# Performance work log

Measured on AMD Instinct MI355X. Metric: run time of the kernel, lower is better.

Reference implementation:

```python
import jax, jax.numpy as jnp
import numpy as np

B, D, K, A, P = 4096, 512, 128, 32, 16  # batch, theta dim, mixture comps, alpha dim, hutchinson probes


def setup_inputs() -> dict:
    key = jax.random.key(0)
    k1, k2, k3, k4 = jax.random.split(key, 4)
    thetas = jax.random.normal(k1, (B, D), dtype=jnp.float32)
    alpha = jax.random.normal(k2, (K, A), dtype=jnp.float32)
    W = jax.random.normal(k3, (A, D), dtype=jnp.float32) / jnp.sqrt(jnp.float32(A))
    v_int = jax.random.randint(k4, (P, B, D), 0, 2, dtype=jnp.int32)  # -> Rademacher via 2v-1
    return {"thetas": thetas, "alpha": alpha, "W": W, "v_int": v_int,
            "N_dataset": 100000, "K_alpha_samples": K}


def _log_density(thetas, alpha, W, N_dataset, K_alpha):
    # Tempered Gaussian mixture: mu_k = alpha_k @ W;
    # logp_b = (N/(N+1)) * (logsumexp_k -0.5||theta_b - mu_k||^2 - log K)
    mu = alpha @ W                                        # [K, D]
    # ||t - mu||^2 expanded to avoid a [B,K,D] intermediate
    sq = (jnp.sum(thetas * thetas, -1, keepdims=True)
          - 2.0 * thetas @ mu.T
          + jnp.sum(mu * mu, -1)[None, :])                # [B, K]
    temper = jnp.float32(N_dataset) / (jnp.float32(N_dataset) + 1.0)
    return temper * (jax.nn.logsumexp(-0.5 * sq, axis=1) - jnp.log(jnp.float32(K_alpha)))


def reference(thetas, alpha, W, v_int, N_dataset, K_alpha_samples):
    v = (2 * v_int - 1).astype(thetas.dtype)              # [P, B, D] Rademacher

    def logp_sum(t):
        return jnp.sum(_log_density(t, alpha, W, N_dataset, K_alpha_samples))

    score = jax.grad(logp_sum)                            # gradiente wrt thetas
    g = score(thetas)                                     # [B, D]

    # Hutchinson trace of the per-sample Hessian via forward-over-reverse HVPs,
    # batched over probes (fuses the torch per-probe autograd.grad loop).
    def hvp(vi):
        return jax.jvp(score, (thetas,), (vi,))[1]        # [B, D]

    Hv = jax.vmap(hvp)(v)                                 # [P, B, D]
    traces = jnp.mean(jnp.sum(v * Hv, axis=-1), axis=0)   # [B]

    loss = 0.5 * jnp.sum(g * g, axis=-1) + traces         # [B]
    return jnp.mean(loss)
```

## Files before the change

kernel.cpp:

```cpp
#include <hip/hip_runtime.h>
#include <hip/hip_bf16.h>
#include <stdint.h>

#define Bsz 4096
#define Dn  512
#define Kn  128
#define Pn  16
#define An  32
#define TB  16

typedef __attribute__((ext_vector_type(4))) float  floatx4;
typedef __attribute__((ext_vector_type(8))) short  shortx8;

__device__ unsigned short g_mu_bf[Kn * Dn];
__device__ unsigned short g_mu_t[Dn * Kn];
__device__ float          g_munorm[Kn];
__device__ float          g_w[Bsz * Kn];

__device__ __forceinline__ unsigned short f2bf(float x) {
    union { float f; uint32_t u; } v; v.f = x;
    uint32_t u = v.u;
    uint32_t r = (u + 0x7FFFu + ((u >> 16) & 1u)) >> 16;
    return (unsigned short)r;
}

__device__ __forceinline__ float rowsum16(float x) {
    x += __int_as_float(__builtin_amdgcn_update_dpp(0, __float_as_int(x), 0xB1, 0xF, 0xF, false));
    x += __int_as_float(__builtin_amdgcn_update_dpp(0, __float_as_int(x), 0x4E, 0xF, 0xF, false));
    x += __int_as_float(__builtin_amdgcn_update_dpp(0, __float_as_int(x), 0x124, 0xF, 0xF, false));
    x += __int_as_float(__builtin_amdgcn_update_dpp(0, __float_as_int(x), 0x128, 0xF, 0xF, false));
    return x;
}

__global__ __launch_bounds__(256) void k_mu(const float* __restrict__ alpha,
                                            const float* __restrict__ W,
                                            float* __restrict__ out) {
    __shared__ float al[An];
    __shared__ float red[4];
    int k = blockIdx.x, t = threadIdx.x;
    if (k == 0 && t == 0) *out = 0.f;
    if (t < An) al[t] = alpha[k * An + t];
    __syncthreads();
    int d0 = t, d1 = t + 256;
    float a0 = 0.f, a1 = 0.f;
#pragma unroll
    for (int a = 0; a < An; ++a) {
        float av = al[a];
        a0 = fmaf(av, W[a * Dn + d0], a0);
        a1 = fmaf(av, W[a * Dn + d1], a1);
    }
    unsigned short h0 = f2bf(a0), h1 = f2bf(a1);
    g_mu_bf[k * Dn + d0] = h0;  g_mu_bf[k * Dn + d1] = h1;
    g_mu_t[d0 * Kn + k] = h0;   g_mu_t[d1 * Kn + k] = h1;
    float nrm = a0 * a0 + a1 * a1;
#pragma unroll
    for (int msk = 1; msk < 64; msk <<= 1) nrm += __shfl_xor(nrm, msk);
    if ((t & 63) == 0) red[t >> 6] = nrm;
    __syncthreads();
    if (t == 0) g_munorm[k] = red[0] + red[1] + red[2] + red[3];
}

__global__ __launch_bounds__(512) void k_w(const float* __restrict__ thetas,
                                           const int* __restrict__ Np,
                                           float* __restrict__ out) {
    __shared__ short vt[TB][520];
    __shared__ float S_l[TB][132];
    __shared__ float w_l[TB][132];
    __shared__ short wbf[TB][136];
    __shared__ float part8[8][TB];
    __shared__ float thn[TB];
    __shared__ float SwS[TB];

    const int tid = threadIdx.x;
    const int lane = tid & 63;
    const int wv = tid >> 6;
    const int m = lane & 15;
    const int q = lane >> 4;
    const int b0 = blockIdx.x * TB;

    const float Nf = (float)(*Np);
    const float temper = Nf / (Nf + 1.0f);

    const int kcol = wv * 16 + m;
    shortx8 mufrag[16];
    {
        const unsigned short* mb = g_mu_bf + (size_t)kcol * Dn + q * 8;
#pragma unroll
        for (int dc = 0; dc < 16; ++dc)
            mufrag[dc] = *(const shortx8*)(mb + dc * 32);
    }

    const int r = tid >> 5;
    const int c0 = (tid & 31) * 16;
    {
        const float4* tg = (const float4*)(thetas + (size_t)(b0 + r) * Dn + c0);
        float tn = 0.f;
#pragma unroll
        for (int j = 0; j < 4; ++j) {
            float4 f = tg[j];
            tn += f.x * f.x + f.y * f.y + f.z * f.z + f.w * f.w;
            short4 h;
            h.x = (short)f2bf(f.x); h.y = (short)f2bf(f.y);
            h.z = (short)f2bf(f.z); h.w = (short)f2bf(f.w);
            *(short4*)&vt[r][c0 + j * 4] = h;
        }
#pragma unroll
        for (int msk = 1; msk < 32; msk <<= 1) tn += __shfl_xor(tn, msk);
        if ((tid & 31) == 0) thn[r] = tn;
    }
    __syncthreads();

    {
        floatx4 acc = {0.f, 0.f, 0.f, 0.f};
#pragma unroll
        for (int dc = 0; dc < 16; ++dc) {
            shortx8 a = *(const shortx8*)&vt[m][dc * 32 + q * 8];
            acc = __builtin_amdgcn_mfma_f32_16x16x32_bf16(a, mufrag[dc], acc, 0, 0, 0);
        }
#pragma unroll
        for (int i = 0; i < 4; ++i) S_l[q * 4 + i][kcol] = acc[i];
    }
    __syncthreads();

    {
        const int b = tid >> 5, s = tid & 31;
        float l[4];
        float mx = -3.4e38f;
        float tnb = thn[b];
#pragma unroll
        for (int j = 0; j < 4; ++j) {
            int k = s + 32 * j;
            l[j] = -0.5f * (tnb - 2.f * S_l[b][k] + g_munorm[k]);
            mx = fmaxf(mx, l[j]);
        }
#pragma unroll
        for (int msk = 1; msk < 32; msk <<= 1) mx = fmaxf(mx, __shfl_xor(mx, msk));
        float se = 0.f, ses = 0.f;
        float e[4];
#pragma unroll
        for (int j = 0; j < 4; ++j) {
            int k = s + 32 * j;
            e[j] = __expf(l[j] - mx);
            se += e[j];
            ses += e[j] * S_l[b][k];
        }
#pragma unroll
        for (int msk = 1; msk < 32; msk <<= 1) { se += __shfl_xor(se, msk); ses += __shfl_xor(ses, msk); }
        float inv = 1.f / se;
#pragma unroll
        for (int j = 0; j < 4; ++j) {
            int k = s + 32 * j;
            float wvv = e[j] * inv;
            w_l[b][k] = wvv;
            wbf[b][k] = (short)f2bf(wvv);
            g_w[(size_t)(b0 + b) * Kn + k] = wvv;
        }
        if (s == 0) SwS[b] = ses * inv;
    }
    __syncthreads();

    {
        float sg[4] = {0.f, 0.f, 0.f, 0.f};
#pragma unroll
        for (int ct = 0; ct < 4; ++ct) {
            const unsigned short* mt = g_mu_t + (size_t)(wv * 64 + ct * 16 + m) * Kn + q * 8;
            floatx4 acc = {0.f, 0.f, 0.f, 0.f};
#pragma unroll
            for (int kc = 0; kc < 4; ++kc) {
                shortx8 a = *(const shortx8*)&wbf[m][kc * 32 + q * 8];
                shortx8 bfr = *(const shortx8*)(mt + kc * 32);
                acc = __builtin_amdgcn_mfma_f32_16x16x32_bf16(a, bfr, acc, 0, 0, 0);
            }
#pragma unroll
            for (int i = 0; i < 4; ++i) sg[i] += acc[i] * acc[i];
        }
#pragma unroll
        for (int i = 0; i < 4; ++i) sg[i] = rowsum16(sg[i]);
        if (m == 0) {
#pragma unroll
            for (int i = 0; i < 4; ++i) part8[wv][q * 4 + i] = sg[i];
        }
    }
    __syncthreads();

    if (tid < TB) {
        float wGw = 0.f;
#pragma unroll
        for (int w8 = 0; w8 < 8; ++w8) wGw += part8[w8][tid];
        float res = 0.5f * temper * temper * (wGw - 2.f * SwS[tid] + thn[tid])
                    - temper * (float)Dn;
#pragma unroll
        for (int msk = 1; msk < 16; msk <<= 1) res += __shfl_xor(res, msk);
        if (tid == 0) atomicAdd(out, res * (1.0f / (float)Bsz));
    }
}

__global__ __launch_bounds__(1024, 4) void k_probe(const int* __restrict__ v_int,
                                                   const int* __restrict__ Np,
                                                   float* __restrict__ out) {
    __shared__ __align__(16) unsigned short mu_l[Kn * Dn];
    __shared__ float w_l[TB][132];
    __shared__ float partial[16];

    const int tid = threadIdx.x;
    const int lane = tid & 63;
    const int wv = tid >> 6;
    const int m = lane & 15;
    const int q = lane >> 4;
    const int bt = blockIdx.x;
    const int r0 = bt * TB;

    const float Nf = (float)(*Np);
    const float temper = Nf / (Nf + 1.0f);

    {
        const int4* src = (const int4*)g_mu_bf;
#pragma unroll
        for (int i = 0; i < 8; ++i) {
            int c = i * 1024 + tid;
            int row = c >> 6;
            int off = (c & 63) * 16;
            int4 val = src[c];
            *(int4*)((char*)mu_l + row * 1024 + (off ^ ((row & 7) << 4))) = val;
        }
    }
    if (tid < 512) {
        int row = tid >> 5, c = (tid & 31) * 4;
        float4 w4 = *(const float4*)(g_w + (size_t)(r0 + row) * Kn + c);
        *(float4*)&w_l[row][c] = w4;
    }
    __syncthreads();

    const size_t PB = (size_t)Bsz * Dn;
    const char* vg = (const char*)(v_int + (size_t)wv * PB + (size_t)(r0 + m) * Dn) + q * 32;

    int4 vb[4][2];
#pragma unroll
    for (int c = 0; c < 4; ++c) {
        vb[c][0] = *(const int4*)(vg + c * 128);
        vb[c][1] = *(const int4*)(vg + c * 128 + 16);
    }

    floatx4 acc[8];
#pragma unroll
    for (int kt = 0; kt < 8; ++kt) acc[kt] = (floatx4){0.f, 0.f, 0.f, 0.f};

    const int swz = (m & 7) << 4;
#pragma unroll
    for (int dc = 0; dc < 16; ++dc) {
        int4 w0 = vb[dc & 3][0], w1 = vb[dc & 3][1];
        if (dc < 12) {
            vb[dc & 3][0] = *(const int4*)(vg + (dc + 4) * 128);
            vb[dc & 3][1] = *(const int4*)(vg + (dc + 4) * 128 + 16);
        }
        union { uint32_t u[4]; shortx8 s; } af;
        af.u[0] = 0xBF80BF80u ^ ((uint32_t)w0.x << 15) ^ ((uint32_t)w0.y << 31);
        af.u[1] = 0xBF80BF80u ^ ((uint32_t)w0.z << 15) ^ ((uint32_t)w0.w << 31);
        af.u[2] = 0xBF80BF80u ^ ((uint32_t)w1.x << 15) ^ ((uint32_t)w1.y << 31);
        af.u[3] = 0xBF80BF80u ^ ((uint32_t)w1.z << 15) ^ ((uint32_t)w1.w << 31);
        const int boff = dc * 64 + q * 16;
#pragma unroll
        for (int kt = 0; kt < 8; ++kt) {
            shortx8 bf = *(const shortx8*)((const char*)mu_l
                              + (kt * 16 + m) * 1024 + (boff ^ swz));
            acc[kt] = __builtin_amdgcn_mfma_f32_16x16x32_bf16(af.s, bf, acc[kt], 0, 0, 0);
        }
    }

    float contrib = 0.f;
#pragma unroll
    for (int i = 0; i < 4; ++i) {
        float s1 = 0.f, s2 = 0.f;
#pragma unroll
        for (int kt = 0; kt < 8; ++kt) {
            float T = acc[kt][i];
            float ww = w_l[q * 4 + i][kt * 16 + m];
            s1 = fmaf(ww * T, T, s1);
            s2 = fmaf(ww, T, s2);
        }
        s1 = rowsum16(s1);
        s2 = rowsum16(s2);
        contrib += s1 - s2 * s2;
    }
    if (m != 0) contrib = 0.f;
    contrib += __shfl_xor(contrib, 16);
    contrib += __shfl_xor(contrib, 32);
    if (lane == 0) partial[wv] = contrib;
    __syncthreads();
    if (tid == 0) {
        float t = 0.f;
#pragma unroll
        for (int i = 0; i < 16; ++i) t += partial[i];
        atomicAdd(out, t * temper * (1.0f / (float)Pn) * (1.0f / (float)Bsz));
    }
}

extern "C" void kernel_launch(void* const* d_in, const int* in_sizes, int n_in,
                              void* d_out, int out_size, void* d_ws, size_t ws_size,
                              hipStream_t stream) {
    const float* thetas = (const float*)d_in[0];
    const float* alpha  = (const float*)d_in[1];
    const float* W      = (const float*)d_in[2];
    const int*   v_int  = (const int*)d_in[3];
    const int*   Np     = (const int*)d_in[4];
    (void)d_ws; (void)ws_size;

    float* out = (float*)d_out;
    k_mu   <<<dim3(Kn),  dim3(256),  0, stream>>>(alpha, W, out);
    k_w    <<<dim3(256), dim3(512),  0, stream>>>(thetas, Np, out);
    k_probe<<<dim3(256), dim3(1024), 0, stream>>>(v_int, Np, out);
}
```

Before: 223.2 us.

## Fuse mixture-weight kernel into probe kernel and deepen v_int prefetch

Merges the k_w kernel, which computes softmax weights, the score norm and the mean term, into k_probe. The fused kernel reuses the mu tile already staged in shared memory instead of reading it again from global memory, and drops the global g_w round trip and one kernel launch. The v_int prefetch depth grows from 4 to 6 chunks and is issued before the weight computation, so its latency overlaps that work. The cost is higher register pressure under the 1024-thread, 4-block launch bounds, and half the waves sit idle during the fused weight phase.

```diff
diff --git a/kernel.cpp b/kernel.cpp
--- a/kernel.cpp
+++ b/kernel.cpp
@@ -15,7 +15,6 @@
 __device__ unsigned short g_mu_bf[Kn * Dn];
 __device__ unsigned short g_mu_t[Dn * Kn];
 __device__ float          g_munorm[Kn];
-__device__ float          g_w[Bsz * Kn];
 
 __device__ __forceinline__ unsigned short f2bf(float x) {
     union { float f; uint32_t u; } v; v.f = x;
@@ -60,146 +59,17 @@
     if (t == 0) g_munorm[k] = red[0] + red[1] + red[2] + red[3];
 }
 
-__global__ __launch_bounds__(512) void k_w(const float* __restrict__ thetas,
-                                           const int* __restrict__ Np,
-                                           float* __restrict__ out) {
-    __shared__ short vt[TB][520];
+__global__ __launch_bounds__(1024, 4) void k_probe(const float* __restrict__ thetas,
+                                                   const int* __restrict__ v_int,
+                                                   const int* __restrict__ Np,
+                                                   float* __restrict__ out) {
+    __shared__ __align__(16) unsigned short mu_l[Kn * Dn];
     __shared__ float S_l[TB][132];
     __shared__ float w_l[TB][132];
     __shared__ short wbf[TB][136];
     __shared__ float part8[8][TB];
     __shared__ float thn[TB];
     __shared__ float SwS[TB];
-
-    const int tid = threadIdx.x;
-    const int lane = tid & 63;
-    const int wv = tid >> 6;
-    const int m = lane & 15;
-    const int q = lane >> 4;
-    const int b0 = blockIdx.x * TB;
-
-    const float Nf = (float)(*Np);
-    const float temper = Nf / (Nf + 1.0f);
-
-    const int kcol = wv * 16 + m;
-    shortx8 mufrag[16];
-    {
-        const unsigned short* mb = g_mu_bf + (size_t)kcol * Dn + q * 8;
-#pragma unroll
-        for (int dc = 0; dc < 16; ++dc)
-            mufrag[dc] = *(const shortx8*)(mb + dc * 32);
-    }
-
-    const int r = tid >> 5;
-    const int c0 = (tid & 31) * 16;
-    {
-        const float4* tg = (const float4*)(thetas + (size_t)(b0 + r) * Dn + c0);
-        float tn = 0.f;
-#pragma unroll
-        for (int j = 0; j < 4; ++j) {
-            float4 f = tg[j];
-            tn += f.x * f.x + f.y * f.y + f.z * f.z + f.w * f.w;
-            short4 h;
-            h.x = (short)f2bf(f.x); h.y = (short)f2bf(f.y);
-            h.z = (short)f2bf(f.z); h.w = (short)f2bf(f.w);
-            *(short4*)&vt[r][c0 + j * 4] = h;
-        }
-#pragma unroll
-        for (int msk = 1; msk < 32; msk <<= 1) tn += __shfl_xor(tn, msk);
-        if ((tid & 31) == 0) thn[r] = tn;
-    }
-    __syncthreads();
-
-    {
-        floatx4 acc = {0.f, 0.f, 0.f, 0.f};
-#pragma unroll
-        for (int dc = 0; dc < 16; ++dc) {
-            shortx8 a = *(const shortx8*)&vt[m][dc * 32 + q * 8];
-            acc = __builtin_amdgcn_mfma_f32_16x16x32_bf16(a, mufrag[dc], acc, 0, 0, 0);
-        }
-#pragma unroll
-        for (int i = 0; i < 4; ++i) S_l[q * 4 + i][kcol] = acc[i];
-    }
-    __syncthreads();
-
-    {
-        const int b = tid >> 5, s = tid & 31;
-        float l[4];
-        float mx = -3.4e38f;
-        float tnb = thn[b];
-#pragma unroll
-        for (int j = 0; j < 4; ++j) {
-            int k = s + 32 * j;
-            l[j] = -0.5f * (tnb - 2.f * S_l[b][k] + g_munorm[k]);
-            mx = fmaxf(mx, l[j]);
-        }
-#pragma unroll
-        for (int msk = 1; msk < 32; msk <<= 1) mx = fmaxf(mx, __shfl_xor(mx, msk));
-        float se = 0.f, ses = 0.f;
-        float e[4];
-#pragma unroll
-        for (int j = 0; j < 4; ++j) {
-            int k = s + 32 * j;
-            e[j] = __expf(l[j] - mx);
-            se += e[j];
-            ses += e[j] * S_l[b][k];
-        }
-#pragma unroll
-        for (int msk = 1; msk < 32; msk <<= 1) { se += __shfl_xor(se, msk); ses += __shfl_xor(ses, msk); }
-        float inv = 1.f / se;
-#pragma unroll
-        for (int j = 0; j < 4; ++j) {
-            int k = s + 32 * j;
-            float wvv = e[j] * inv;
-            w_l[b][k] = wvv;
-            wbf[b][k] = (short)f2bf(wvv);
-            g_w[(size_t)(b0 + b) * Kn + k] = wvv;
-        }
-        if (s == 0) SwS[b] = ses * inv;
-    }
-    __syncthreads();
-
-    {
-        float sg[4] = {0.f, 0.f, 0.f, 0.f};
-#pragma unroll
-        for (int ct = 0; ct < 4; ++ct) {
-            const unsigned short* mt = g_mu_t + (size_t)(wv * 64 + ct * 16 + m) * Kn + q * 8;
-            floatx4 acc = {0.f, 0.f, 0.f, 0.f};
-#pragma unroll
-            for (int kc = 0; kc < 4; ++kc) {
-                shortx8 a = *(const shortx8*)&wbf[m][kc * 32 + q * 8];
-                shortx8 bfr = *(const shortx8*)(mt + kc * 32);
-                acc = __builtin_amdgcn_mfma_f32_16x16x32_bf16(a, bfr, acc, 0, 0, 0);
-            }
-#pragma unroll
-            for (int i = 0; i < 4; ++i) sg[i] += acc[i] * acc[i];
-        }
-#pragma unroll
-        for (int i = 0; i < 4; ++i) sg[i] = rowsum16(sg[i]);
-        if (m == 0) {
-#pragma unroll
-            for (int i = 0; i < 4; ++i) part8[wv][q * 4 + i] = sg[i];
-        }
-    }
-    __syncthreads();
-
-    if (tid < TB) {
-        float wGw = 0.f;
-#pragma unroll
-        for (int w8 = 0; w8 < 8; ++w8) wGw += part8[w8][tid];
-        float res = 0.5f * temper * temper * (wGw - 2.f * SwS[tid] + thn[tid])
-                    - temper * (float)Dn;
-#pragma unroll
-        for (int msk = 1; msk < 16; msk <<= 1) res += __shfl_xor(res, msk);
-        if (tid == 0) atomicAdd(out, res * (1.0f / (float)Bsz));
-    }
-}
-
-__global__ __launch_bounds__(1024, 4) void k_probe(const int* __restrict__ v_int,
-                                                   const int* __restrict__ Np,
-                                                   float* __restrict__ out) {
-    __shared__ __align__(16) unsigned short mu_l[Kn * Dn];
-    __shared__ float w_l[TB][132];
     __shared__ float partial[16];
 
     const int tid = threadIdx.x;
@@ -212,6 +82,7 @@
 
     const float Nf = (float)(*Np);
     const float temper = Nf / (Nf + 1.0f);
+    const int swz = (m & 7) << 4;
 
     {
         const int4* src = (const int4*)g_mu_bf;
@@ -224,34 +95,125 @@
             *(int4*)((char*)mu_l + row * 1024 + (off ^ ((row & 7) << 4))) = val;
         }
     }
-    if (tid < 512) {
-        int row = tid >> 5, c = (tid & 31) * 4;
-        float4 w4 = *(const float4*)(g_w + (size_t)(r0 + row) * Kn + c);
-        *(float4*)&w_l[row][c] = w4;
-    }
-    __syncthreads();
 
     const size_t PB = (size_t)Bsz * Dn;
     const char* vg = (const char*)(v_int + (size_t)wv * PB + (size_t)(r0 + m) * Dn) + q * 32;
-
-    int4 vb[4][2];
-#pragma unroll
-    for (int c = 0; c < 4; ++c) {
+    int4 vb[6][2];
+#pragma unroll
+    for (int c = 0; c < 6; ++c) {
         vb[c][0] = *(const int4*)(vg + c * 128);
         vb[c][1] = *(const int4*)(vg + c * 128 + 16);
     }
+    __syncthreads();
+
+    if (wv < 8) {
+        const float* tg = thetas + (size_t)(r0 + m) * Dn + q * 8;
+        floatx4 acc = {0.f, 0.f, 0.f, 0.f};
+        float tn = 0.f;
+#pragma unroll
+        for (int dc = 0; dc < 16; ++dc) {
+            float4 f0 = *(const float4*)(tg + dc * 32);
+            float4 f1 = *(const float4*)(tg + dc * 32 + 4);
+            tn += f0.x * f0.x + f0.y * f0.y + f0.z * f0.z + f0.w * f0.w
+                + f1.x * f1.x + f1.y * f1.y + f1.z * f1.z + f1.w * f1.w;
+            union { uint32_t u[4]; shortx8 s; } af;
+            af.u[0] = (uint32_t)f2bf(f0.x) | ((uint32_t)f2bf(f0.y) << 16);
+            af.u[1] = (uint32_t)f2bf(f0.z) | ((uint32_t)f2bf(f0.w) << 16);
+            af.u[2] = (uint32_t)f2bf(f1.x) | ((uint32_t)f2bf(f1.y) << 16);
+            af.u[3] = (uint32_t)f2bf(f1.z) | ((uint32_t)f2bf(f1.w) << 16);
+            shortx8 bf = *(const shortx8*)((const char*)mu_l
+                              + (wv * 16 + m) * 1024 + ((dc * 64 + q * 16) ^ swz));
+            acc = __builtin_amdgcn_mfma_f32_16x16x32_bf16(af.s, bf, acc, 0, 0, 0);
+        }
+#pragma unroll
+        for (int i = 0; i < 4; ++i) S_l[q * 4 + i][wv * 16 + m] = acc[i];
+        tn += __shfl_xor(tn, 16);
+        tn += __shfl_xor(tn, 32);
+        if (wv == 0 && q == 0) thn[m] = tn;
+    }
+    __syncthreads();
+
+    if (tid < 512) {
+        const int b = tid >> 5, s = tid & 31;
+        float l[4];
+        float mx = -3.4e38f;
+        float tnb = thn[b];
+#pragma unroll
+        for (int j = 0; j < 4; ++j) {
+            int k = s + 32 * j;
+            l[j] = -0.5f * (tnb - 2.f * S_l[b][k] + g_munorm[k]);
+            mx = fmaxf(mx, l[j]);
+        }
+#pragma unroll
+        for (int msk = 1; msk < 32; msk <<= 1) mx = fmaxf(mx, __shfl_xor(mx, msk));
+        float se = 0.f, ses = 0.f;
+        float e[4];
+#pragma unroll
+        for (int j = 0; j < 4; ++j) {
+            int k = s + 32 * j;
+            e[j] = __expf(l[j] - mx);
+            se += e[j];
+            ses += e[j] * S_l[b][k];
+        }
+#pragma unroll
+        for (int msk = 1; msk < 32; msk <<= 1) { se += __shfl_xor(se, msk); ses += __shfl_xor(ses, msk); }
+        float inv = 1.f / se;
+#pragma unroll
+        for (int j = 0; j < 4; ++j) {
+            int k = s + 32 * j;
+            float wvv = e[j] * inv;
+            w_l[b][k] = wvv;
+            wbf[b][k] = (short)f2bf(wvv);
+        }
+        if (s == 0) SwS[b] = ses * inv;
+    }
+    __syncthreads();
+
+    if (wv < 8) {
+        float sg[4] = {0.f, 0.f, 0.f, 0.f};
+#pragma unroll
+        for (int ct = 0; ct < 4; ++ct) {
+            const unsigned short* mt = g_mu_t + (size_t)(wv * 64 + ct * 16 + m) * Kn + q * 8;
+            floatx4 acc = {0.f, 0.f, 0.f, 0.f};
+#pragma unroll
+            for (int kc = 0; kc < 4; ++kc) {
+                shortx8 a = *(const shortx8*)&wbf[m][kc * 32 + q * 8];
+                shortx8 bfr = *(const shortx8*)(mt + kc * 32);
+                acc = __builtin_amdgcn_mfma_f32_16x16x32_bf16(a, bfr, acc, 0, 0, 0);
+            }
+#pragma unroll
+            for (int i = 0; i < 4; ++i) sg[i] += acc[i] * acc[i];
+        }
+#pragma unroll
+        for (int i = 0; i < 4; ++i) sg[i] = rowsum16(sg[i]);
+        if (m == 0) {
+#pragma unroll
+            for (int i = 0; i < 4; ++i) part8[wv][q * 4 + i] = sg[i];
+        }
+    }
+    __syncthreads();
+
+    if (tid < TB) {
+        float wGw = 0.f;
+#pragma unroll
+        for (int w8 = 0; w8 < 8; ++w8) wGw += part8[w8][tid];
+        float res = 0.5f * temper * temper * (wGw - 2.f * SwS[tid] + thn[tid])
+                    - temper * (float)Dn;
+#pragma unroll
+        for (int msk = 1; msk < 16; msk <<= 1) res += __shfl_xor(res, msk);
+        if (tid == 0) atomicAdd(out, res * (1.0f / (float)Bsz));
+    }
 
     floatx4 acc[8];
 #pragma unroll
     for (int kt = 0; kt < 8; ++kt) acc[kt] = (floatx4){0.f, 0.f, 0.f, 0.f};
 
-    const int swz = (m & 7) << 4;
 #pragma unroll
     for (int dc = 0; dc < 16; ++dc) {
-        int4 w0 = vb[dc & 3][0], w1 = vb[dc & 3][1];
-        if (dc < 12) {
-            vb[dc & 3][0] = *(const int4*)(vg + (dc + 4) * 128);
-            vb[dc & 3][1] = *(const int4*)(vg + (dc + 4) * 128 + 16);
+        int4 w0 = vb[dc % 6][0], w1 = vb[dc % 6][1];
+        if (dc < 10) {
+            vb[dc % 6][0] = *(const int4*)(vg + (dc + 6) * 128);
+            vb[dc % 6][1] = *(const int4*)(vg + (dc + 6) * 128 + 16);
         }
         union { uint32_t u[4]; shortx8 s; } af;
         af.u[0] = 0xBF80BF80u ^ ((uint32_t)w0.x << 15) ^ ((uint32_t)w0.y << 31);
@@ -307,6 +269,5 @@
 
     float* out = (float*)d_out;
     k_mu   <<<dim3(Kn),  dim3(256),  0, stream>>>(alpha, W, out);
-    k_w    <<<dim3(256), dim3(512),  0, stream>>>(thetas, Np, out);
-    k_probe<<<dim3(256), dim3(1024), 0, stream>>>(v_int, Np, out);
-}
+    k_probe<<<dim3(256), dim3(1024), 0, stream>>>(thetas, v_int, Np, out);
+}
```

Measured after the change: 245.1 us. 9.8% more time.
